# Kernel optimization log

Hardware: AMD Instinct MI355X
Metric: run time of the kernel (lower is better)

The kernel has to match this reference:

```python
import jax, jax.numpy as jnp
import numpy as np

NUM_USERS = 100000
NUM_ITEMS = 50000
EMB = 64
N_LAYERS = 3
NNZ = 4800000
N_NODES = NUM_USERS + NUM_ITEMS


def setup_inputs() -> dict:
    key = jax.random.key(0)
    k1, k2, k3, k4, k5 = jax.random.split(key, 5)
    emb_user = jax.random.normal(k1, (NUM_USERS, EMB), dtype=jnp.float32) * 0.1
    emb_item = jax.random.normal(k2, (NUM_ITEMS, EMB), dtype=jnp.float32) * 0.1
    adj_rows = jax.random.randint(k3, (NNZ,), 0, N_NODES, dtype=jnp.int32)
    adj_cols = jax.random.randint(k4, (NNZ,), 0, N_NODES, dtype=jnp.int32)
    # normalized adjacency values (stand-in for D^-1/2 A D^-1/2 entries)
    adj_vals = jax.random.uniform(k5, (NNZ,), dtype=jnp.float32) / 32.0
    return {
        "emb_user": emb_user,
        "emb_item": emb_item,
        "adj_vals": adj_vals,
        "adj_rows": adj_rows,
        "adj_cols": adj_cols,
    }


def _spmm(vals, rows, cols, x):
    # y[r] = sum_{e: rows[e]==r} vals[e] * x[cols[e]]
    gathered = x[cols] * vals[:, None]  # [nnz, emb]
    return jax.ops.segment_sum(gathered, rows, num_segments=N_NODES)


def reference(emb_user, emb_item, adj_vals, adj_rows, adj_cols):
    ego = jnp.concatenate([emb_user, emb_item], axis=0)  # [(U+I), emb]
    acc = ego
    h = ego
    for _ in range(N_LAYERS):
        h = _spmm(adj_vals, adj_rows, adj_cols, h)
        acc = acc + h
    mean_emb = acc / jnp.float32(N_LAYERS + 1)
    user_embeddings = mean_emb[:NUM_USERS]
    item_embeddings = mean_emb[NUM_USERS:]
    return user_embeddings, item_embeddings
```

## Files before the change

### kernel.cpp

```cpp
#include <hip/hip_runtime.h>
#include <hip/hip_bf16.h>

#define N_USERS   100000
#define N_ITEMS   50000
#define N_NODES_C 150000
#define EMB       64
#define N_ELEM    (N_NODES_C * EMB)
#define BKT_SHIFT 9
#define NBKT      ((N_NODES_C + 511) >> 9)
#define BKT_CAP   20480
#define CH_EDGES  4096
#define EPT       16

typedef unsigned int u32x4 __attribute__((ext_vector_type(4)));

__global__ void detect_and_zero(const unsigned int* __restrict__ emb_u32,
                                const unsigned int* __restrict__ vals_u32,
                                int* __restrict__ flags,
                                int* __restrict__ tails) {
    int t = threadIdx.x;
    for (int b = t; b < NBKT; b += 256) tails[b] = 0;
    int cnt_emb = 0, cnt_vals = 0;
    for (int k = t; k < 1024; k += 256) {
        unsigned e = (emb_u32[k] >> 7) & 0xFFu;
        cnt_emb += (e >= 100u && e <= 127u) ? 1 : 0;
        cnt_vals += (vals_u32[k] >> 15) & 1u;
    }
    __shared__ int s0[256], s1[256];
    s0[t] = cnt_emb; s1[t] = cnt_vals;
    __syncthreads();
    for (int s = 128; s > 0; s >>= 1) {
        if (t < s) { s0[t] += s0[t + s]; s1[t] += s1[t + s]; }
        __syncthreads();
    }
    if (t == 0) {
        flags[0] = (s0[0] > 512) ? 1 : 0;
        flags[1] = (s1[0] > 100) ? 0 : 1;
    }
}

__device__ __forceinline__ float load_f(const void* base, size_t i, int is_bf16) {
    if (is_bf16) return __bfloat162float(((const __hip_bfloat16*)base)[i]);
    return ((const float*)base)[i];
}
__device__ __forceinline__ unsigned int bf16_bits(float f) {
    __hip_bfloat16 h = __float2bfloat16(f);
    return (unsigned int)reinterpret_cast<unsigned short&>(h);
}
__device__ __forceinline__ float lo_bf(unsigned int u) {
    return __uint_as_float(u << 16);
}
__device__ __forceinline__ float hi_bf(unsigned int u) {
    return __uint_as_float(u & 0xFFFF0000u);
}

__global__ void init_kernel(const void* __restrict__ eu,
                            const void* __restrict__ ei,
                            __hip_bfloat16* __restrict__ h0,
                            const int* __restrict__ flags) {
    int i = blockIdx.x * blockDim.x + threadIdx.x;
    if (i >= N_ELEM) return;
    int ebf = flags[0];
    float f = (i < N_USERS * EMB) ? load_f(eu, i, ebf)
                                  : load_f(ei, i - N_USERS * EMB, ebf);
    h0[i] = __float2bfloat16(f);
}

__global__ void scatter_bucket(const int* __restrict__ rows, const int* __restrict__ cols,
                               const void* __restrict__ vals,
                               unsigned long long* __restrict__ tmp,
                               int* __restrict__ tails, int nnz,
                               const int* __restrict__ flags) {
    __shared__ int lcnt[NBKT];
    __shared__ int lbase[NBKT];
    int t = threadIdx.x;
    for (int b = t; b < NBKT; b += 256) lcnt[b] = 0;
    __syncthreads();
    int base = blockIdx.x * CH_EDGES;
    int vbf = flags[1];
    unsigned long long pk[EPT];
    unsigned int br[EPT];
    #pragma unroll
    for (int i = 0; i < EPT; ++i) {
        int e = base + i * 256 + t;
        if (e < nnz) {
            int r = rows[e];
            int c = cols[e];
            float v = load_f(vals, (size_t)e, vbf);
            int bk = r >> BKT_SHIFT;
            int rk = atomicAdd(&lcnt[bk], 1);
            pk[i] = ((unsigned long long)(unsigned)r << 34)
                  | ((unsigned long long)(unsigned)c << 16)
                  | (unsigned long long)bf16_bits(v);
            br[i] = ((unsigned)bk << 16) | (unsigned)rk;
        } else {
            br[i] = 0xFFFFFFFFu;
        }
    }
    __syncthreads();
    for (int b = t; b < NBKT; b += 256)
        lbase[b] = lcnt[b] ? atomicAdd(&tails[b], lcnt[b]) : 0;
    __syncthreads();
    #pragma unroll
    for (int i = 0; i < EPT; ++i) {
        if (br[i] != 0xFFFFFFFFu) {
            int bk = br[i] >> 16, rk = br[i] & 0xFFFFu;
            int pos = lbase[bk] + rk;
            if (pos < BKT_CAP)
                tmp[(size_t)bk * BKT_CAP + pos] = pk[i];
        }
    }
}

__global__ void scan_bkt(const int* __restrict__ tails, int* __restrict__ bktbase) {
    __shared__ int l[512];
    int t = threadIdx.x;
    int v = (t < NBKT) ? tails[t] : 0;
    l[t] = v;
    __syncthreads();
    for (int off = 1; off < 512; off <<= 1) {
        int u = (t >= off) ? l[t - off] : 0;
        __syncthreads();
        l[t] += u;
        __syncthreads();
    }
    if (t < NBKT) bktbase[t] = l[t] - v;
    if (t == NBKT - 1) bktbase[NBKT] = l[t];
}

__global__ void bucket_csr(const unsigned long long* __restrict__ tmp,
                           int2* __restrict__ edges,
                           const int* __restrict__ tails,
                           const int* __restrict__ bktbase,
                           int* __restrict__ row_ptr) {
    __shared__ int cnt[512];
    __shared__ int off[512];
    int b = blockIdx.x, t = threadIdx.x;
    int rowbase = b << BKT_SHIFT;
    int nrows = N_NODES_C - rowbase; if (nrows > 512) nrows = 512;
    int n = tails[b];
    if (n > BKT_CAP) n = BKT_CAP;
    const unsigned long long* src = tmp + (size_t)b * BKT_CAP;
    int obase = bktbase[b];
    cnt[t] = 0;
    __syncthreads();
    for (int e = t; e < n; e += 512)
        atomicAdd(&cnt[(int)(src[e] >> 34) - rowbase], 1);
    __syncthreads();
    int v = cnt[t];
    off[t] = v;
    __syncthreads();
    for (int o = 1; o < 512; o <<= 1) {
        int u = (t >= o) ? off[t - o] : 0;
        __syncthreads();
        off[t] += u;
        __syncthreads();
    }
    int excl = off[t] - v;
    __syncthreads();
    off[t] = obase + excl;
    if (t < nrows) row_ptr[rowbase + t] = obase + excl;
    if (b == NBKT - 1 && t == 0) row_ptr[N_NODES_C] = obase + n;
    __syncthreads();
    for (int e = t; e < n; e += 512) {
        unsigned long long p = src[e];
        int rloc = (int)(p >> 34) - rowbase;
        int c = (int)((p >> 16) & 0x3FFFFu);
        int pos = atomicAdd(&off[rloc], 1);
        edges[pos] = make_int2(c, (int)((unsigned)(p & 0xFFFFu) << 16));
    }
}

#define ACC8(v, g)                      \
    a0 += (v) * lo_bf((g).x);           \
    a1 += (v) * hi_bf((g).x);           \
    a2 += (v) * lo_bf((g).y);           \
    a3 += (v) * hi_bf((g).y);           \
    a4 += (v) * lo_bf((g).z);           \
    a5 += (v) * hi_bf((g).z);           \
    a6 += (v) * lo_bf((g).w);           \
    a7 += (v) * hi_bf((g).w);

__global__ void spmm8(const __hip_bfloat16* __restrict__ x,
                      __hip_bfloat16* __restrict__ y,
                      const unsigned long long* __restrict__ edges,
                      const int* __restrict__ row_ptr,
                      const __hip_bfloat16* __restrict__ h0,
                      const __hip_bfloat16* __restrict__ h1,
                      void* __restrict__ out,
                      const int* __restrict__ flags,
                      int last) {
    int row = blockIdx.x * 4 + (threadIdx.x >> 6);
    if (row >= N_NODES_C) return;
    int lane = threadIdx.x & 63;
    int slot = lane >> 3;
    int s    = lane & 7;
    int beg = row_ptr[row], end = row_ptr[row + 1];
    float a0 = 0.f, a1 = 0.f, a2 = 0.f, a3 = 0.f,
          a4 = 0.f, a5 = 0.f, a6 = 0.f, a7 = 0.f;
    for (int e = beg; e < end; e += 32) {
        int iA = e + slot;
        int iB = iA + 8;
        int iC = iA + 16;
        int iD = iA + 24;
        unsigned long long pA = (iA < end) ? __builtin_nontemporal_load(edges + iA) : 0ULL;
        unsigned long long pB = (iB < end) ? __builtin_nontemporal_load(edges + iB) : 0ULL;
        unsigned long long pC = (iC < end) ? __builtin_nontemporal_load(edges + iC) : 0ULL;
        unsigned long long pD = (iD < end) ? __builtin_nontemporal_load(edges + iD) : 0ULL;
        const uint4 gA = *reinterpret_cast<const uint4*>(
            x + ((size_t)(unsigned)(pA & 0xFFFFFFFFu) << 6) + (s << 3));
        const uint4 gB = *reinterpret_cast<const uint4*>(
            x + ((size_t)(unsigned)(pB & 0xFFFFFFFFu) << 6) + (s << 3));
        const uint4 gC = *reinterpret_cast<const uint4*>(
            x + ((size_t)(unsigned)(pC & 0xFFFFFFFFu) << 6) + (s << 3));
        const uint4 gD = *reinterpret_cast<const uint4*>(
            x + ((size_t)(unsigned)(pD & 0xFFFFFFFFu) << 6) + (s << 3));
        float vA = __uint_as_float((unsigned)(pA >> 32));
        float vB = __uint_as_float((unsigned)(pB >> 32));
        float vC = __uint_as_float((unsigned)(pC >> 32));
        float vD = __uint_as_float((unsigned)(pD >> 32));
        ACC8(vA, gA);
        ACC8(vB, gB);
        ACC8(vC, gC);
        ACC8(vD, gD);
    }
    #pragma unroll
    for (int m = 8; m < 64; m <<= 1) {
        a0 += __shfl_xor(a0, m, 64);
        a1 += __shfl_xor(a1, m, 64);
        a2 += __shfl_xor(a2, m, 64);
        a3 += __shfl_xor(a3, m, 64);
        a4 += __shfl_xor(a4, m, 64);
        a5 += __shfl_xor(a5, m, 64);
        a6 += __shfl_xor(a6, m, 64);
        a7 += __shfl_xor(a7, m, 64);
    }
    if (slot != 0) return;
    size_t base = ((size_t)row << 6) + (s << 3);
    if (!last) {
        u32x4 o;
        o.x = bf16_bits(a0) | (bf16_bits(a1) << 16);
        o.y = bf16_bits(a2) | (bf16_bits(a3) << 16);
        o.z = bf16_bits(a4) | (bf16_bits(a5) << 16);
        o.w = bf16_bits(a6) | (bf16_bits(a7) << 16);
        __builtin_nontemporal_store(o, reinterpret_cast<u32x4*>(y + base));
    } else {
        const uint4 r0 = *reinterpret_cast<const uint4*>(h0 + base);
        const uint4 r1 = *reinterpret_cast<const uint4*>(h1 + base);
        const uint4 r2 = *reinterpret_cast<const uint4*>(x + base);
        float f0 = (lo_bf(r0.x) + lo_bf(r1.x) + lo_bf(r2.x) + a0) * 0.25f;
        float f1 = (hi_bf(r0.x) + hi_bf(r1.x) + hi_bf(r2.x) + a1) * 0.25f;
        float f2 = (lo_bf(r0.y) + lo_bf(r1.y) + lo_bf(r2.y) + a2) * 0.25f;
        float f3 = (hi_bf(r0.y) + hi_bf(r1.y) + hi_bf(r2.y) + a3) * 0.25f;
        float f4 = (lo_bf(r0.z) + lo_bf(r1.z) + lo_bf(r2.z) + a4) * 0.25f;
        float f5 = (hi_bf(r0.z) + hi_bf(r1.z) + hi_bf(r2.z) + a5) * 0.25f;
        float f6 = (lo_bf(r0.w) + lo_bf(r1.w) + lo_bf(r2.w) + a6) * 0.25f;
        float f7 = (hi_bf(r0.w) + hi_bf(r1.w) + hi_bf(r2.w) + a7) * 0.25f;
        if (flags[0]) {
            u32x4 o;
            o.x = bf16_bits(f0) | (bf16_bits(f1) << 16);
            o.y = bf16_bits(f2) | (bf16_bits(f3) << 16);
            o.z = bf16_bits(f4) | (bf16_bits(f5) << 16);
            o.w = bf16_bits(f6) | (bf16_bits(f7) << 16);
            __builtin_nontemporal_store(
                o, reinterpret_cast<u32x4*>((__hip_bfloat16*)out + base));
        } else {
            float* op = (float*)out + base;
            u32x4 q0, q1;
            q0.x = __float_as_uint(f0); q0.y = __float_as_uint(f1);
            q0.z = __float_as_uint(f2); q0.w = __float_as_uint(f3);
            q1.x = __float_as_uint(f4); q1.y = __float_as_uint(f5);
            q1.z = __float_as_uint(f6); q1.w = __float_as_uint(f7);
            __builtin_nontemporal_store(q0, reinterpret_cast<u32x4*>(op));
            __builtin_nontemporal_store(q1, reinterpret_cast<u32x4*>(op + 4));
        }
    }
}

extern "C" void kernel_launch(void* const* d_in, const int* in_sizes, int n_in,
                              void* d_out, int out_size, void* d_ws, size_t ws_size,
                              hipStream_t stream) {
    const void* eu   = d_in[0];
    const void* ei   = d_in[1];
    const void* vals = d_in[2];
    const int*  rows = (const int*)d_in[3];
    const int*  cols = (const int*)d_in[4];
    const int nnz = in_sizes[2];

    __hip_bfloat16* h[3];
    h[0] = (__hip_bfloat16*)d_ws;
    h[1] = h[0] + N_ELEM;
    h[2] = h[1] + N_ELEM;
    int2* edges   = (int2*)(h[2] + N_ELEM);
    int* row_ptr  = (int*)(edges + nnz);
    int* bktbase  = row_ptr + (N_NODES_C + 1);
    int* tails    = bktbase + (NBKT + 1);
    int* flags    = tails + NBKT;
    char* pt = (char*)(flags + 2);
    unsigned long long* tmp =
        (unsigned long long*)(((uintptr_t)pt + 7) & ~(uintptr_t)7);

    detect_and_zero<<<1, 256, 0, stream>>>((const unsigned int*)eu,
                                           (const unsigned int*)vals, flags, tails);
    init_kernel<<<(N_ELEM + 255) / 256, 256, 0, stream>>>(eu, ei, h[0], flags);

    int nchunks = (nnz + CH_EDGES - 1) / CH_EDGES;
    scatter_bucket<<<nchunks, 256, 0, stream>>>(rows, cols, vals, tmp, tails, nnz, flags);
    scan_bkt<<<1, 512, 0, stream>>>(tails, bktbase);
    bucket_csr<<<NBKT, 512, 0, stream>>>(tmp, edges, tails, bktbase, row_ptr);

    int nsb = (N_NODES_C + 3) / 4;
    spmm8<<<nsb, 256, 0, stream>>>(h[0], h[1], (const unsigned long long*)edges, row_ptr,
                                   nullptr, nullptr, nullptr, flags, 0);
    spmm8<<<nsb, 256, 0, stream>>>(h[1], h[2], (const unsigned long long*)edges, row_ptr,
                                   nullptr, nullptr, nullptr, flags, 0);
    spmm8<<<nsb, 256, 0, stream>>>(h[2], nullptr, (const unsigned long long*)edges, row_ptr,
                                   h[0], h[1], d_out, flags, 1);
}
```

Baseline: 518.2 us.

## Fold bucket scan into CSR build and use dot2 bf16 math in SpMM

Removes the separate bucket-scan launch; each bucket_csr block now computes its own prefix by summing earlier bucket tails in shared memory. Edge column indices are prestored as byte offsets (c<<7), so the SpMM skips the shift/multiply in address computation. Inner accumulation switches to packed v_dot2_f32_bf16 with byte-permute pairing of two edges' values. The cross-lane reduction uses ds_swizzle for the first two steps, output packing uses v_cvt_pk_bf16_f32, and the row index is made wave-uniform via readfirstlane. The intent is fewer instructions and launches, at the cost of redundant prefix work per block and a change in rounding order.

```diff
diff --git a/kernel.cpp b/kernel.cpp
--- a/kernel.cpp
+++ b/kernel.cpp
@@ -13,6 +13,7 @@
 #define EPT       16
 
 typedef unsigned int u32x4 __attribute__((ext_vector_type(4)));
+typedef unsigned long long u64;
 
 __global__ void detect_and_zero(const unsigned int* __restrict__ emb_u32,
                                 const unsigned int* __restrict__ vals_u32,
@@ -68,7 +69,7 @@
 
 __global__ void scatter_bucket(const int* __restrict__ rows, const int* __restrict__ cols,
                                const void* __restrict__ vals,
-                               unsigned long long* __restrict__ tmp,
+                               u64* __restrict__ tmp,
                                int* __restrict__ tails, int nnz,
                                const int* __restrict__ flags) {
     __shared__ int lcnt[NBKT];
@@ -78,7 +79,7 @@
     __syncthreads();
     int base = blockIdx.x * CH_EDGES;
     int vbf = flags[1];
-    unsigned long long pk[EPT];
+    u64 pk[EPT];
     unsigned int br[EPT];
     #pragma unroll
     for (int i = 0; i < EPT; ++i) {
@@ -89,9 +90,9 @@
             float v = load_f(vals, (size_t)e, vbf);
             int bk = r >> BKT_SHIFT;
             int rk = atomicAdd(&lcnt[bk], 1);
-            pk[i] = ((unsigned long long)(unsigned)r << 34)
-                  | ((unsigned long long)(unsigned)c << 16)
-                  | (unsigned long long)bf16_bits(v);
+            pk[i] = ((u64)(unsigned)r << 34)
+                  | ((u64)(unsigned)c << 16)
+                  | (u64)bf16_bits(v);
             br[i] = ((unsigned)bk << 16) | (unsigned)rk;
         } else {
             br[i] = 0xFFFFFFFFu;
@@ -112,38 +113,32 @@
     }
 }
 
-__global__ void scan_bkt(const int* __restrict__ tails, int* __restrict__ bktbase) {
-    __shared__ int l[512];
-    int t = threadIdx.x;
-    int v = (t < NBKT) ? tails[t] : 0;
-    l[t] = v;
-    __syncthreads();
-    for (int off = 1; off < 512; off <<= 1) {
-        int u = (t >= off) ? l[t - off] : 0;
-        __syncthreads();
-        l[t] += u;
-        __syncthreads();
-    }
-    if (t < NBKT) bktbase[t] = l[t] - v;
-    if (t == NBKT - 1) bktbase[NBKT] = l[t];
-}
-
-__global__ void bucket_csr(const unsigned long long* __restrict__ tmp,
+__global__ void bucket_csr(const u64* __restrict__ tmp,
                            int2* __restrict__ edges,
                            const int* __restrict__ tails,
-                           const int* __restrict__ bktbase,
                            int* __restrict__ row_ptr) {
     __shared__ int cnt[512];
     __shared__ int off[512];
+    __shared__ int red[512];
     int b = blockIdx.x, t = threadIdx.x;
+    int pre = 0;
+    for (int i = t; i < b; i += 512) {
+        int v = tails[i];
+        pre += (v > BKT_CAP) ? BKT_CAP : v;
+    }
+    red[t] = pre;
+    cnt[t] = 0;
     int rowbase = b << BKT_SHIFT;
     int nrows = N_NODES_C - rowbase; if (nrows > 512) nrows = 512;
     int n = tails[b];
     if (n > BKT_CAP) n = BKT_CAP;
-    const unsigned long long* src = tmp + (size_t)b * BKT_CAP;
-    int obase = bktbase[b];
-    cnt[t] = 0;
-    __syncthreads();
+    const u64* src = tmp + (size_t)b * BKT_CAP;
+    __syncthreads();
+    for (int st = 256; st > 0; st >>= 1) {
+        if (t < st) red[t] += red[t + st];
+        __syncthreads();
+    }
+    int obase = red[0];
     for (int e = t; e < n; e += 512)
         atomicAdd(&cnt[(int)(src[e] >> 34) - rowbase], 1);
     __syncthreads();
@@ -163,86 +158,95 @@
     if (b == NBKT - 1 && t == 0) row_ptr[N_NODES_C] = obase + n;
     __syncthreads();
     for (int e = t; e < n; e += 512) {
-        unsigned long long p = src[e];
+        u64 p = src[e];
         int rloc = (int)(p >> 34) - rowbase;
-        int c = (int)((p >> 16) & 0x3FFFFu);
+        unsigned c = (unsigned)((p >> 16) & 0x3FFFFu);
         int pos = atomicAdd(&off[rloc], 1);
-        edges[pos] = make_int2(c, (int)((unsigned)(p & 0xFFFFu) << 16));
-    }
-}
-
-#define ACC8(v, g)                      \
-    a0 += (v) * lo_bf((g).x);           \
-    a1 += (v) * hi_bf((g).x);           \
-    a2 += (v) * lo_bf((g).y);           \
-    a3 += (v) * hi_bf((g).y);           \
-    a4 += (v) * lo_bf((g).z);           \
-    a5 += (v) * hi_bf((g).z);           \
-    a6 += (v) * lo_bf((g).w);           \
-    a7 += (v) * hi_bf((g).w);
+        edges[pos] = make_int2((int)(c << 7), (int)((unsigned)(p & 0xFFFFu) << 16));
+    }
+}
+
+#define DOT2Q(wA, wB, vp, ae, ao)                                              \
+    {                                                                          \
+        unsigned _xe = __builtin_amdgcn_perm((wA), (wB), 0x01000504u);         \
+        unsigned _xo = __builtin_amdgcn_perm((wA), (wB), 0x03020706u);         \
+        asm("v_dot2_f32_bf16 %0, %1, %2, %0" : "+v"(ae) : "v"(_xe), "v"(vp));  \
+        asm("v_dot2_f32_bf16 %0, %1, %2, %0" : "+v"(ao) : "v"(_xo), "v"(vp));  \
+    }
+
+#define SWZ_ADD(a, pat) \
+    a += __int_as_float(__builtin_amdgcn_ds_swizzle(__float_as_int(a), pat))
 
 __global__ void spmm8(const __hip_bfloat16* __restrict__ x,
                       __hip_bfloat16* __restrict__ y,
-                      const unsigned long long* __restrict__ edges,
+                      const u64* __restrict__ edges,
                       const int* __restrict__ row_ptr,
                       const __hip_bfloat16* __restrict__ h0,
                       const __hip_bfloat16* __restrict__ h1,
                       void* __restrict__ out,
                       const int* __restrict__ flags,
                       int last) {
-    int row = blockIdx.x * 4 + (threadIdx.x >> 6);
+    int row = __builtin_amdgcn_readfirstlane(blockIdx.x * 4 + (threadIdx.x >> 6));
     if (row >= N_NODES_C) return;
     int lane = threadIdx.x & 63;
     int slot = lane >> 3;
     int s    = lane & 7;
     int beg = row_ptr[row], end = row_ptr[row + 1];
+    const char* xb = (const char*)x;
+    const char* eb = (const char*)edges;
+    unsigned s16 = (unsigned)s << 4;
+    unsigned eoff = ((unsigned)(beg + slot)) << 3;
     float a0 = 0.f, a1 = 0.f, a2 = 0.f, a3 = 0.f,
           a4 = 0.f, a5 = 0.f, a6 = 0.f, a7 = 0.f;
-    for (int e = beg; e < end; e += 32) {
-        int iA = e + slot;
-        int iB = iA + 8;
-        int iC = iA + 16;
-        int iD = iA + 24;
-        unsigned long long pA = (iA < end) ? __builtin_nontemporal_load(edges + iA) : 0ULL;
-        unsigned long long pB = (iB < end) ? __builtin_nontemporal_load(edges + iB) : 0ULL;
-        unsigned long long pC = (iC < end) ? __builtin_nontemporal_load(edges + iC) : 0ULL;
-        unsigned long long pD = (iD < end) ? __builtin_nontemporal_load(edges + iD) : 0ULL;
-        const uint4 gA = *reinterpret_cast<const uint4*>(
-            x + ((size_t)(unsigned)(pA & 0xFFFFFFFFu) << 6) + (s << 3));
-        const uint4 gB = *reinterpret_cast<const uint4*>(
-            x + ((size_t)(unsigned)(pB & 0xFFFFFFFFu) << 6) + (s << 3));
-        const uint4 gC = *reinterpret_cast<const uint4*>(
-            x + ((size_t)(unsigned)(pC & 0xFFFFFFFFu) << 6) + (s << 3));
-        const uint4 gD = *reinterpret_cast<const uint4*>(
-            x + ((size_t)(unsigned)(pD & 0xFFFFFFFFu) << 6) + (s << 3));
-        float vA = __uint_as_float((unsigned)(pA >> 32));
-        float vB = __uint_as_float((unsigned)(pB >> 32));
-        float vC = __uint_as_float((unsigned)(pC >> 32));
-        float vD = __uint_as_float((unsigned)(pD >> 32));
-        ACC8(vA, gA);
-        ACC8(vB, gB);
-        ACC8(vC, gC);
-        ACC8(vD, gD);
-    }
-    #pragma unroll
-    for (int m = 8; m < 64; m <<= 1) {
-        a0 += __shfl_xor(a0, m, 64);
-        a1 += __shfl_xor(a1, m, 64);
-        a2 += __shfl_xor(a2, m, 64);
-        a3 += __shfl_xor(a3, m, 64);
-        a4 += __shfl_xor(a4, m, 64);
-        a5 += __shfl_xor(a5, m, 64);
-        a6 += __shfl_xor(a6, m, 64);
-        a7 += __shfl_xor(a7, m, 64);
-    }
+    for (int e = beg; e < end; e += 32, eoff += 256) {
+        int rem = end - e;
+        const u64* ep = (const u64*)(eb + eoff);
+        u64 pA = (slot      < rem) ? __builtin_nontemporal_load(ep)      : 0ULL;
+        u64 pB = (slot + 8  < rem) ? __builtin_nontemporal_load(ep + 8)  : 0ULL;
+        u64 pC = (slot + 16 < rem) ? __builtin_nontemporal_load(ep + 16) : 0ULL;
+        u64 pD = (slot + 24 < rem) ? __builtin_nontemporal_load(ep + 24) : 0ULL;
+        unsigned oA = (unsigned)pA + s16;
+        unsigned oB = (unsigned)pB + s16;
+        unsigned oC = (unsigned)pC + s16;
+        unsigned oD = (unsigned)pD + s16;
+        const uint4 gA = *reinterpret_cast<const uint4*>(xb + oA);
+        const uint4 gB = *reinterpret_cast<const uint4*>(xb + oB);
+        const uint4 gC = *reinterpret_cast<const uint4*>(xb + oC);
+        const uint4 gD = *reinterpret_cast<const uint4*>(xb + oD);
+        unsigned vAB = __builtin_amdgcn_perm((unsigned)(pA >> 32),
+                                             (unsigned)(pB >> 32), 0x03020706u);
+        unsigned vCD = __builtin_amdgcn_perm((unsigned)(pC >> 32),
+                                             (unsigned)(pD >> 32), 0x03020706u);
+        DOT2Q(gA.x, gB.x, vAB, a0, a1);
+        DOT2Q(gA.y, gB.y, vAB, a2, a3);
+        DOT2Q(gA.z, gB.z, vAB, a4, a5);
+        DOT2Q(gA.w, gB.w, vAB, a6, a7);
+        DOT2Q(gC.x, gD.x, vCD, a0, a1);
+        DOT2Q(gC.y, gD.y, vCD, a2, a3);
+        DOT2Q(gC.z, gD.z, vCD, a4, a5);
+        DOT2Q(gC.w, gD.w, vCD, a6, a7);
+    }
+    SWZ_ADD(a0, 0x201F); SWZ_ADD(a1, 0x201F); SWZ_ADD(a2, 0x201F); SWZ_ADD(a3, 0x201F);
+    SWZ_ADD(a4, 0x201F); SWZ_ADD(a5, 0x201F); SWZ_ADD(a6, 0x201F); SWZ_ADD(a7, 0x201F);
+    SWZ_ADD(a0, 0x401F); SWZ_ADD(a1, 0x401F); SWZ_ADD(a2, 0x401F); SWZ_ADD(a3, 0x401F);
+    SWZ_ADD(a4, 0x401F); SWZ_ADD(a5, 0x401F); SWZ_ADD(a6, 0x401F); SWZ_ADD(a7, 0x401F);
+    a0 += __shfl_xor(a0, 32, 64);
+    a1 += __shfl_xor(a1, 32, 64);
+    a2 += __shfl_xor(a2, 32, 64);
+    a3 += __shfl_xor(a3, 32, 64);
+    a4 += __shfl_xor(a4, 32, 64);
+    a5 += __shfl_xor(a5, 32, 64);
+    a6 += __shfl_xor(a6, 32, 64);
+    a7 += __shfl_xor(a7, 32, 64);
     if (slot != 0) return;
     size_t base = ((size_t)row << 6) + (s << 3);
     if (!last) {
-        u32x4 o;
-        o.x = bf16_bits(a0) | (bf16_bits(a1) << 16);
-        o.y = bf16_bits(a2) | (bf16_bits(a3) << 16);
-        o.z = bf16_bits(a4) | (bf16_bits(a5) << 16);
-        o.w = bf16_bits(a6) | (bf16_bits(a7) << 16);
+        unsigned q0, q1, q2, q3;
+        asm("v_cvt_pk_bf16_f32 %0, %1, %2" : "=v"(q0) : "v"(a0), "v"(a1));
+        asm("v_cvt_pk_bf16_f32 %0, %1, %2" : "=v"(q1) : "v"(a2), "v"(a3));
+        asm("v_cvt_pk_bf16_f32 %0, %1, %2" : "=v"(q2) : "v"(a4), "v"(a5));
+        asm("v_cvt_pk_bf16_f32 %0, %1, %2" : "=v"(q3) : "v"(a6), "v"(a7));
+        u32x4 o; o.x = q0; o.y = q1; o.z = q2; o.w = q3;
         __builtin_nontemporal_store(o, reinterpret_cast<u32x4*>(y + base));
     } else {
         const uint4 r0 = *reinterpret_cast<const uint4*>(h0 + base);
@@ -257,11 +261,12 @@
         float f6 = (lo_bf(r0.w) + lo_bf(r1.w) + lo_bf(r2.w) + a6) * 0.25f;
         float f7 = (hi_bf(r0.w) + hi_bf(r1.w) + hi_bf(r2.w) + a7) * 0.25f;
         if (flags[0]) {
-            u32x4 o;
-            o.x = bf16_bits(f0) | (bf16_bits(f1) << 16);
-            o.y = bf16_bits(f2) | (bf16_bits(f3) << 16);
-            o.z = bf16_bits(f4) | (bf16_bits(f5) << 16);
-            o.w = bf16_bits(f6) | (bf16_bits(f7) << 16);
+            unsigned q0, q1, q2, q3;
+            asm("v_cvt_pk_bf16_f32 %0, %1, %2" : "=v"(q0) : "v"(f0), "v"(f1));
+            asm("v_cvt_pk_bf16_f32 %0, %1, %2" : "=v"(q1) : "v"(f2), "v"(f3));
+            asm("v_cvt_pk_bf16_f32 %0, %1, %2" : "=v"(q2) : "v"(f4), "v"(f5));
+            asm("v_cvt_pk_bf16_f32 %0, %1, %2" : "=v"(q3) : "v"(f6), "v"(f7));
+            u32x4 o; o.x = q0; o.y = q1; o.z = q2; o.w = q3;
             __builtin_nontemporal_store(
                 o, reinterpret_cast<u32x4*>((__hip_bfloat16*)out + base));
         } else {
@@ -293,12 +298,10 @@
     h[2] = h[1] + N_ELEM;
     int2* edges   = (int2*)(h[2] + N_ELEM);
     int* row_ptr  = (int*)(edges + nnz);
-    int* bktbase  = row_ptr + (N_NODES_C + 1);
-    int* tails    = bktbase + (NBKT + 1);
+    int* tails    = row_ptr + (N_NODES_C + 1);
     int* flags    = tails + NBKT;
     char* pt = (char*)(flags + 2);
-    unsigned long long* tmp =
-        (unsigned long long*)(((uintptr_t)pt + 7) & ~(uintptr_t)7);
+    u64* tmp = (u64*)(((uintptr_t)pt + 7) & ~(uintptr_t)7);
 
     detect_and_zero<<<1, 256, 0, stream>>>((const unsigned int*)eu,
                                            (const unsigned int*)vals, flags, tails);
@@ -306,14 +309,13 @@
 
     int nchunks = (nnz + CH_EDGES - 1) / CH_EDGES;
     scatter_bucket<<<nchunks, 256, 0, stream>>>(rows, cols, vals, tmp, tails, nnz, flags);
-    scan_bkt<<<1, 512, 0, stream>>>(tails, bktbase);
-    bucket_csr<<<NBKT, 512, 0, stream>>>(tmp, edges, tails, bktbase, row_ptr);
+    bucket_csr<<<NBKT, 512, 0, stream>>>(tmp, edges, tails, row_ptr);
 
     int nsb = (N_NODES_C + 3) / 4;
-    spmm8<<<nsb, 256, 0, stream>>>(h[0], h[1], (const unsigned long long*)edges, row_ptr,
+    spmm8<<<nsb, 256, 0, stream>>>(h[0], h[1], (const u64*)edges, row_ptr,
                                    nullptr, nullptr, nullptr, flags, 0);
-    spmm8<<<nsb, 256, 0, stream>>>(h[1], h[2], (const unsigned long long*)edges, row_ptr,
+    spmm8<<<nsb, 256, 0, stream>>>(h[1], h[2], (const u64*)edges, row_ptr,
                                    nullptr, nullptr, nullptr, flags, 0);
-    spmm8<<<nsb, 256, 0, stream>>>(h[2], nullptr, (const unsigned long long*)edges, row_ptr,
+    spmm8<<<nsb, 256, 0, stream>>>(h[2], nullptr, (const u64*)edges, row_ptr,
                                    h[0], h[1], d_out, flags, 1);
 }
```

Result: no change. 510.0 us (-1.6%).
